# Kernel optimization log

Hardware: AMD Instinct MI355X
Metric: run time of the kernel (lower is better)

The kernel has to match this reference:

```python
import jax, jax.numpy as jnp
import numpy as np

B, IN, MEM, CTX, H = 8192, 1024, 1024, 1024, 4
DH = CTX // H

def setup_inputs() -> dict:
    key = jax.random.key(0)
    ks = jax.random.split(key, 20)
    s = 0.02
    d = {
        'input_tensor': jax.random.normal(ks[0], (B, IN), jnp.float32),
        'previous_memory': jax.random.normal(ks[1], (B, MEM), jnp.float32),
        # MultiheadAttention packed in_proj (q,k,v) and out_proj
        'in_proj_w': jax.random.normal(ks[2], (3 * CTX, CTX), jnp.float32) * s,
        'in_proj_b': jnp.zeros((3 * CTX,), jnp.float32),
        'out_proj_w': jax.random.normal(ks[3], (CTX, CTX), jnp.float32) * s,
        'out_proj_b': jnp.zeros((CTX,), jnp.float32),
        # input/memory projections
        'ip_w': jax.random.normal(ks[4], (CTX, IN), jnp.float32) * s,
        'ip_b': jnp.zeros((CTX,), jnp.float32),
        'mp_w': jax.random.normal(ks[5], (CTX, MEM), jnp.float32) * s,
        'mp_b': jnp.zeros((CTX,), jnp.float32),
        # forget / output gates
        'fg_w': jax.random.normal(ks[6], (MEM, MEM + IN), jnp.float32) * s,
        'fg_b': jnp.zeros((MEM,), jnp.float32),
        'og_w': jax.random.normal(ks[7], (MEM, MEM), jnp.float32) * s,
        'og_b': jnp.zeros((MEM,), jnp.float32),
        # GRUCell weights (PyTorch layout: [3*hidden, in], gates order r,z,n)
        'gru_w_ih': jax.random.normal(ks[8], (3 * MEM, CTX), jnp.float32) * s,
        'gru_b_ih': jnp.zeros((3 * MEM,), jnp.float32),
        'gru_w_hh': jax.random.normal(ks[9], (3 * MEM, MEM), jnp.float32) * s,
        'gru_b_hh': jnp.zeros((3 * MEM,), jnp.float32),
    }
    return d

def _forward(input_tensor, previous_memory, in_proj_w, in_proj_b, out_proj_w, out_proj_b,
             ip_w, ip_b, mp_w, mp_b, fg_w, fg_b, og_w, og_b,
             gru_w_ih, gru_b_ih, gru_w_hh, gru_b_hh):
    # projections
    pi = input_tensor @ ip_w.T + ip_b          # [B, CTX] (query; also context/value)
    pm = previous_memory @ mp_w.T + mp_b       # [B, CTX] (key)
    # MHA with q_len = kv_len = 1: softmax over a single key -> weights = 1
    wq, wk, wv = jnp.split(in_proj_w, 3, axis=0)
    bq, bk, bv = jnp.split(in_proj_b, 3, axis=0)
    q = (pi @ wq.T + bq).reshape(B, H, DH)
    k = (pm @ wk.T + bk).reshape(B, H, DH)
    v = (pi @ wv.T + bv).reshape(B, H, DH)
    scores = jnp.sum(q * k, axis=-1, keepdims=True) / jnp.sqrt(jnp.float32(DH))  # [B,H,1]
    w = jax.nn.softmax(scores, axis=-1)        # all ones (single key)
    attn = (w * v).reshape(B, CTX)             # == v
    context_aware = attn @ out_proj_w.T + out_proj_b  # [B, CTX]
    attention_weights = jnp.mean(w, axis=1)[:, None, :]  # [B,1,1], avg over heads
    # forget gate
    forget_in = jnp.concatenate([previous_memory, input_tensor], axis=-1)
    fgate = jax.nn.sigmoid(forget_in @ fg_w.T + fg_b)
    gated_mem = previous_memory * fgate
    # GRUCell (PyTorch semantics)
    gi = context_aware @ gru_w_ih.T + gru_b_ih
    gh = gated_mem @ gru_w_hh.T + gru_b_hh
    gi_r, gi_z, gi_n = jnp.split(gi, 3, axis=-1)
    gh_r, gh_z, gh_n = jnp.split(gh, 3, axis=-1)
    r = jax.nn.sigmoid(gi_r + gh_r)
    z = jax.nn.sigmoid(gi_z + gh_z)
    n = jnp.tanh(gi_n + r * gh_n)
    updated = (1.0 - z) * n + z * gated_mem
    ogate = jax.nn.sigmoid(updated @ og_w.T + og_b)
    return updated * ogate, attention_weights

def reference(input_tensor, previous_memory, in_proj_w, in_proj_b, out_proj_w, out_proj_b,
              ip_w, ip_b, mp_w, mp_b, fg_w, fg_b, og_w, og_b,
              gru_w_ih, gru_b_ih, gru_w_hh, gru_b_hh):
    return _forward(input_tensor, previous_memory, in_proj_w, in_proj_b, out_proj_w, out_proj_b,
                    ip_w, ip_b, mp_w, mp_b, fg_w, fg_b, og_w, og_b,
                    gru_w_ih, gru_b_ih, gru_w_hh, gru_b_hh)
```

## Files before the change

### kernel.cpp

```cpp
#include <hip/hip_runtime.h>
#include <cstdint>
#include <cstddef>


typedef __bf16 bf16;
typedef bf16 bf16x4 __attribute__((ext_vector_type(4)));
typedef bf16 bf16x8 __attribute__((ext_vector_type(8)));
typedef float f32x4 __attribute__((ext_vector_type(4)));

#define B_ROWS 8192

__device__ __forceinline__ float sigmoid_f(float x) {
    return 1.0f / (1.0f + __expf(-x));
}
__device__ __forceinline__ float tanh_f(float x) {
    return 1.0f - 2.0f / (__expf(2.0f * x) + 1.0f);
}

__global__ __launch_bounds__(256, 2) void gemm256x128_k(
    const bf16* __restrict__ A, int lda,
    const bf16* __restrict__ W, int ldw,
    const float* __restrict__ bias, int N, int K, int epi,
    bf16* __restrict__ out_bf, float* __restrict__ out_f32,
    const float* __restrict__ aux_f32, const bf16* __restrict__ aux_bf,
    int nby)
{
    __shared__ bf16 lds[36864];
    bf16* sA = lds;
    bf16* sB = lds + 3 * 256 * 32;

    const int tid  = threadIdx.x;
    const int lane = tid & 63;
    const int wave = tid >> 6;
    const int wm   = wave >> 1;
    const int wn   = wave & 1;
    const int lrow = lane & 15;
    const int lq   = lane >> 4;

    const int by   = blockIdx.x % nby;
    const int bx   = blockIdx.x / nby;
    const int brow = by * 256;
    const int bcol = bx * 128;

    f32x4 acc[8][4];
#pragma unroll
    for (int i = 0; i < 8; ++i)
#pragma unroll
        for (int j = 0; j < 4; ++j) {
            f32x4 z = {0.0f, 0.0f, 0.0f, 0.0f};
            acc[i][j] = z;
        }

    auto stage = [&](bf16* dA, bf16* dB, int k0) {
#pragma unroll
        for (int i = 0; i < 4; ++i) {
            const int s   = tid + i * 256;
            const int row = s >> 2;
            const int col = (((s & 3) ^ ((s >> 3) & 3)) << 3);
            const bf16* gp = A + (size_t)(brow + row) * lda + (k0 + col);
            __builtin_amdgcn_global_load_lds(
                (const __attribute__((address_space(1))) void*)gp,
                (__attribute__((address_space(3))) void*)(&dA[s * 8]),
                16, 0, 0);
        }
#pragma unroll
        for (int i = 0; i < 2; ++i) {
            const int s   = tid + i * 256;
            const int row = s >> 2;
            const int col = (((s & 3) ^ ((s >> 3) & 3)) << 3);
            const bf16* gp = W + (size_t)(bcol + row) * ldw + (k0 + col);
            __builtin_amdgcn_global_load_lds(
                (const __attribute__((address_space(1))) void*)gp,
                (__attribute__((address_space(3))) void*)(&dB[s * 8]),
                16, 0, 0);
        }
    };

    const int NT = K >> 5;

    bf16* a0 = sA;                bf16* b0 = sB;
    bf16* a1 = sA + 256 * 32;     bf16* b1 = sB + 128 * 32;
    bf16* a2 = sA + 2 * 256 * 32; bf16* b2 = sB + 2 * 128 * 32;

    stage(a0, b0, 0);
    stage(a1, b1, NT > 1 ? 32 : 0);
    asm volatile("s_waitcnt vmcnt(6)" ::: "memory");
    __builtin_amdgcn_s_barrier();
    __builtin_amdgcn_sched_barrier(0);

    for (int kt = 0; kt < NT; ++kt) {
        bf16x8 av[8], bv[4];
#pragma unroll
        for (int i = 0; i < 8; ++i) {
            const int r = wm * 128 + i * 16 + lrow;
            av[i] = *(const bf16x8*)&a0[r * 32 + ((lq ^ ((r >> 1) & 3)) << 3)];
        }
#pragma unroll
        for (int j = 0; j < 4; ++j) {
            const int r = wn * 64 + j * 16 + lrow;
            bv[j] = *(const bf16x8*)&b0[r * 32 + ((lq ^ ((r >> 1) & 3)) << 3)];
        }

        const int kn = (kt + 2 < NT ? kt + 2 : NT - 1) << 5;
        stage(a2, b2, kn);

#pragma unroll
        for (int i = 0; i < 8; ++i)
#pragma unroll
            for (int j = 0; j < 4; ++j)
                acc[i][j] = __builtin_amdgcn_mfma_f32_16x16x32_bf16(
                    av[i], bv[j], acc[i][j], 0, 0, 0);

        __builtin_amdgcn_sched_barrier(0);
        asm volatile("s_waitcnt vmcnt(6)" ::: "memory");
        __builtin_amdgcn_s_barrier();
        __builtin_amdgcn_sched_barrier(0);

        bf16* ta = a0; a0 = a1; a1 = a2; a2 = ta;
        bf16* tb = b0; b0 = b1; b1 = b2; b2 = tb;
    }

    asm volatile("s_waitcnt vmcnt(0)" ::: "memory");
    __syncthreads();

    if (epi == 0) {
        bf16* cb = lds;
#pragma unroll
        for (int j = 0; j < 4; ++j) {
            const int col = wn * 64 + j * 16 + lrow;
            const float bj = bias[bcol + col];
#pragma unroll
            for (int i = 0; i < 8; ++i) {
                const int rowb = wm * 128 + i * 16 + lq * 4;
#pragma unroll
                for (int r = 0; r < 4; ++r)
                    cb[(rowb + r) * 136 + col] = (bf16)(acc[i][j][r] + bj);
            }
        }
        __syncthreads();
#pragma unroll
        for (int p = 0; p < 16; ++p) {
            const int row = p * 16 + (tid >> 4);
            const int col = (tid & 15) * 8;
            bf16x8 v = *(const bf16x8*)&cb[row * 136 + col];
            *(bf16x8*)&out_bf[(size_t)(brow + row) * N + bcol + col] = v;
        }
    } else {
        float* cf = (float*)lds;
#pragma unroll
        for (int h = 0; h < 2; ++h) {
            if (wm == h) {
#pragma unroll
                for (int j = 0; j < 4; ++j) {
                    const int col = wn * 64 + j * 16 + lrow;
                    const float bj = bias[bcol + col];
#pragma unroll
                    for (int i = 0; i < 8; ++i) {
                        const int rl = i * 16 + lq * 4;
#pragma unroll
                        for (int r = 0; r < 4; ++r)
                            cf[(rl + r) * 132 + col] = acc[i][j][r] + bj;
                    }
                }
            }
            __syncthreads();
#pragma unroll
            for (int p = 0; p < 16; ++p) {
                const int idx = p * 256 + tid;
                const int row = idx >> 5;
                const int ch  = idx & 31;
                f32x4 v = *(const f32x4*)&cf[row * 132 + ch * 4];
                const int grow = brow + h * 128 + row;
                const int gcol = bcol + ch * 4;
                const size_t gidx = (size_t)grow * N + gcol;
                if (epi == 1) {
                    f32x4 a4 = *(const f32x4*)&aux_f32[gidx];
                    bf16x4 o;
#pragma unroll
                    for (int e = 0; e < 4; ++e)
                        o[e] = (bf16)(a4[e] * sigmoid_f(v[e]));
                    *(bf16x4*)&out_bf[gidx] = o;
                } else {
                    bf16x4 ab = *(const bf16x4*)&aux_bf[gidx];
                    f32x4 o;
#pragma unroll
                    for (int e = 0; e < 4; ++e)
                        o[e] = (float)ab[e] * sigmoid_f(v[e]);
                    *(f32x4*)&out_f32[gidx] = o;
                }
            }
            __syncthreads();
        }
    }
}

template <int BM>
__device__ __forceinline__ void gemm_core_tb(
    bf16* sA, bf16* sB,
    const bf16* __restrict__ A, int lda,
    const bf16* __restrict__ W, int ldw,
    const float* __restrict__ bias,
    int N, int K, int brow, int bcol, int epi,
    bf16* __restrict__ out_bf, int tld)
{
    constexpr int AI = BM / 32;
    const int tid  = threadIdx.x;
    const int lane = tid & 63;
    const int wave = tid >> 6;
    const int wr   = (wave & 1) * (BM / 2);
    const int wc   = (wave >> 1) * 64;
    const int lrow = lane & 15;
    const int lq   = lane >> 4;

    f32x4 acc[AI][4];
#pragma unroll
    for (int i = 0; i < AI; ++i)
#pragma unroll
        for (int j = 0; j < 4; ++j) {
            f32x4 z = {0.0f, 0.0f, 0.0f, 0.0f};
            acc[i][j] = z;
        }

    auto stage = [&](bf16* dA, bf16* dB, int k0) {
#pragma unroll
        for (int i = 0; i < BM / 64; ++i) {
            const int s   = tid + i * 256;
            const int row = s >> 2;
            const int col = (((s & 3) ^ ((s >> 3) & 3)) << 3);
            const bf16* gp = A + (size_t)(brow + row) * lda + (k0 + col);
            __builtin_amdgcn_global_load_lds(
                (const __attribute__((address_space(1))) void*)gp,
                (__attribute__((address_space(3))) void*)(&dA[s * 8]),
                16, 0, 0);
        }
#pragma unroll
        for (int i = 0; i < 2; ++i) {
            const int s   = tid + i * 256;
            const int row = s >> 2;
            const int col = (((s & 3) ^ ((s >> 3) & 3)) << 3);
            const bf16* gp = W + (size_t)(bcol + row) * ldw + (k0 + col);
            __builtin_amdgcn_global_load_lds(
                (const __attribute__((address_space(1))) void*)gp,
                (__attribute__((address_space(3))) void*)(&dB[s * 8]),
                16, 0, 0);
        }
    };

#define WAIT_LPS()                                                   \
    do {                                                             \
        if constexpr (BM == 128)                                     \
            asm volatile("s_waitcnt vmcnt(4)" ::: "memory");         \
        else                                                         \
            asm volatile("s_waitcnt vmcnt(3)" ::: "memory");         \
    } while (0)

    const int NT = K >> 5;

    bf16* a0 = sA;               bf16* b0 = sB;
    bf16* a1 = sA + BM * 32;     bf16* b1 = sB + 4096;
    bf16* a2 = sA + 2 * BM * 32; bf16* b2 = sB + 2 * 4096;

    stage(a0, b0, 0);
    stage(a1, b1, NT > 1 ? 32 : 0);
    WAIT_LPS();
    __builtin_amdgcn_s_barrier();
    __builtin_amdgcn_sched_barrier(0);

    for (int kt = 0; kt < NT; ++kt) {
        bf16x8 av[AI], bv[4];
#pragma unroll
        for (int i = 0; i < AI; ++i) {
            const int r = wr + i * 16 + lrow;
            av[i] = *(const bf16x8*)&a0[r * 32 + ((lq ^ ((r >> 1) & 3)) << 3)];
        }
#pragma unroll
        for (int j = 0; j < 4; ++j) {
            const int r = wc + j * 16 + lrow;
            bv[j] = *(const bf16x8*)&b0[r * 32 + ((lq ^ ((r >> 1) & 3)) << 3)];
        }

        const int kn = (kt + 2 < NT ? kt + 2 : NT - 1) << 5;
        stage(a2, b2, kn);

#pragma unroll
        for (int i = 0; i < AI; ++i)
#pragma unroll
            for (int j = 0; j < 4; ++j)
                acc[i][j] = __builtin_amdgcn_mfma_f32_16x16x32_bf16(
                    av[i], bv[j], acc[i][j], 0, 0, 0);

        __builtin_amdgcn_sched_barrier(0);
        WAIT_LPS();
        __builtin_amdgcn_s_barrier();
        __builtin_amdgcn_sched_barrier(0);

        bf16* ta = a0; a0 = a1; a1 = a2; a2 = ta;
        bf16* tb = b0; b0 = b1; b1 = b2; b2 = tb;
    }

    asm volatile("s_waitcnt vmcnt(0)" ::: "memory");
#undef WAIT_LPS

#pragma unroll
    for (int j = 0; j < 4; ++j) {
        const int gcol = bcol + wc + j * 16 + lrow;
        const float bj = bias ? bias[gcol] : 0.0f;
#pragma unroll
        for (int i = 0; i < AI; ++i) {
            const int growb = brow + wr + i * 16 + lq * 4;
#pragma unroll
            for (int r = 0; r < 4; ++r) {
                const int grow = growb + r;
                const float val = acc[i][j][r] + bj;
                if (epi == 0) {
                    out_bf[(size_t)grow * N + gcol] = (bf16)val;
                } else {
                    out_bf[(size_t)gcol * tld + grow] = (bf16)val;
                }
            }
        }
    }
}

__global__ __launch_bounds__(256, 2) void gemm64_k(
    const bf16* __restrict__ A, int lda, const bf16* __restrict__ W, int ldw,
    const float* __restrict__ bias, int N, int K, int epi,
    bf16* __restrict__ out_bf, int tld, int nby)
{
    __shared__ bf16 sA[3 * 64 * 32];
    __shared__ bf16 sB[3 * 128 * 32];
    const int by = blockIdx.x % nby;
    const int bx = blockIdx.x / nby;
    gemm_core_tb<64>(sA, sB, A, lda, W, ldw, bias, N, K,
                     by * 64, bx * 128, epi, out_bf, tld);
}


__global__ void cast_weights_k(
    const float* __restrict__ wv, const float* __restrict__ wop,
    const float* __restrict__ wih, const float* __restrict__ wfg,
    const float* __restrict__ wog,
    bf16* __restrict__ dv, bf16* __restrict__ dop, bf16* __restrict__ dih,
    bf16* __restrict__ dfg, bf16* __restrict__ dog)
{
    int c = blockIdx.x * 256 + threadIdx.x;
    const float* s;
    bf16* d;
    int o;
    if (c < 262144)        { s = wv;  d = dv;  o = c; }
    else if (c < 524288)   { s = wop; d = dop; o = c - 262144; }
    else if (c < 1310720)  { s = wih; d = dih; o = c - 524288; }
    else if (c < 1835008)  { s = wfg; d = dfg; o = c - 1310720; }
    else                   { s = wog; d = dog; o = c - 1835008; }
    f32x4 v = ((const f32x4*)s)[o];
    bf16x4 t = {(bf16)v[0], (bf16)v[1], (bf16)v[2], (bf16)v[3]};
    ((bf16x4*)d)[o] = t;
}

__global__ void cast_f32_bf16_k(const float* __restrict__ src,
                                bf16* __restrict__ dst, int n4) {
    int i = blockIdx.x * 256 + threadIdx.x;
    if (i >= n4) return;
    f32x4 v = ((const f32x4*)src)[i];
    bf16x4 o = {(bf16)v[0], (bf16)v[1], (bf16)v[2], (bf16)v[3]};
    ((bf16x4*)dst)[i] = o;
}

__global__ void build_cat_k(const float* __restrict__ mem,
                            const float* __restrict__ inp,
                            bf16* __restrict__ cat) {
    int i = blockIdx.x * 256 + threadIdx.x;
    int row = i >> 9;
    int c4  = i & 511;
    f32x4 v;
    if (c4 < 256)
        v = ((const f32x4*)mem)[(size_t)row * 256 + c4];
    else
        v = ((const f32x4*)inp)[(size_t)row * 256 + (c4 - 256)];
    bf16x4 o = {(bf16)v[0], (bf16)v[1], (bf16)v[2], (bf16)v[3]};
    ((bf16x4*)cat)[i] = o;
}

__global__ void transpose_cast_k(const float* __restrict__ src,
                                 bf16* __restrict__ dst, int R, int C) {
    __shared__ float t[32][33];
    int bx = blockIdx.x * 32;
    int by = blockIdx.y * 32;
    int tx = threadIdx.x & 31, ty = threadIdx.x >> 5;
#pragma unroll
    for (int i = 0; i < 32; i += 8)
        t[ty + i][tx] = src[(size_t)(by + ty + i) * C + bx + tx];
    __syncthreads();
#pragma unroll
    for (int i = 0; i < 32; i += 8)
        dst[(size_t)(bx + ty + i) * R + by + tx] = (bf16)t[tx][ty + i];
}

__global__ void gemv_k(const float* __restrict__ W, const float* __restrict__ x,
                       const float* __restrict__ b, float* __restrict__ y,
                       int K) {
    int n    = blockIdx.x * 4 + (threadIdx.x >> 6);
    int lane = threadIdx.x & 63;
    const float* row = W + (size_t)n * K;
    float s = 0.0f;
    for (int k = lane * 4; k < K; k += 256) {
        f32x4 w = *(const f32x4*)(row + k);
        f32x4 xv = *(const f32x4*)(x + k);
        s += w[0] * xv[0] + w[1] * xv[1] + w[2] * xv[2] + w[3] * xv[3];
    }
#pragma unroll
    for (int off = 32; off; off >>= 1) s += __shfl_down(s, off);
    if (lane == 0) y[n] = s + b[n];
}

__global__ void gru_combine_k(const bf16* __restrict__ gi,
                              const bf16* __restrict__ gh,
                              bf16* __restrict__ gated) {
    int i   = blockIdx.x * 256 + threadIdx.x;
    int row = i >> 7;
    int c   = (i & 127) << 3;
    size_t b3 = (size_t)row * 3072 + c;
    size_t b1 = (size_t)row * 1024 + c;
    bf16x8 gir = *(const bf16x8*)(gi + b3);
    bf16x8 giz = *(const bf16x8*)(gi + b3 + 1024);
    bf16x8 gin = *(const bf16x8*)(gi + b3 + 2048);
    bf16x8 ghr = *(const bf16x8*)(gh + b3);
    bf16x8 ghz = *(const bf16x8*)(gh + b3 + 1024);
    bf16x8 ghn = *(const bf16x8*)(gh + b3 + 2048);
    bf16x8 g   = *(const bf16x8*)(gated + b1);
    bf16x8 o;
#pragma unroll
    for (int e = 0; e < 8; ++e) {
        float r = sigmoid_f((float)gir[e] + (float)ghr[e]);
        float z = sigmoid_f((float)giz[e] + (float)ghz[e]);
        float n = tanh_f((float)gin[e] + r * (float)ghn[e]);
        o[e] = (bf16)((1.0f - z) * n + z * (float)g[e]);
    }
    *(bf16x8*)(gated + b1) = o;
}

__global__ void fill_ones_k(float* __restrict__ p, int n) {
    int i = blockIdx.x * 256 + threadIdx.x;
    if (i < n) p[i] = 1.0f;
}

extern "C" void kernel_launch(void* const* d_in, const int* in_sizes, int n_in,
                              void* d_out, int out_size, void* d_ws,
                              size_t ws_size, hipStream_t stream) {
    const float* input      = (const float*)d_in[0];
    const float* prev       = (const float*)d_in[1];
    const float* in_proj_w  = (const float*)d_in[2];
    const float* in_proj_b  = (const float*)d_in[3];
    const float* out_proj_w = (const float*)d_in[4];
    const float* out_proj_b = (const float*)d_in[5];
    const float* ip_w       = (const float*)d_in[6];
    const float* ip_b       = (const float*)d_in[7];
    const float* fg_w  = (const float*)d_in[10];
    const float* fg_b  = (const float*)d_in[11];
    const float* og_w  = (const float*)d_in[12];
    const float* og_b  = (const float*)d_in[13];
    const float* gih_w = (const float*)d_in[14];
    const float* gih_b = (const float*)d_in[15];
    const float* ghh_w = (const float*)d_in[16];
    const float* ghh_b = (const float*)d_in[17];
    float* out = (float*)d_out;

    char* ws = (char*)d_ws;
    const size_t MB = 1024 * 1024;
    bf16* CAT   = (bf16*)(ws);
    bf16* WHHB  = (bf16*)(ws);
    bf16* GI    = (bf16*)(ws + 32 * MB);
    bf16* GH    = (bf16*)(ws + 80 * MB);
    bf16* WVB   = (bf16*)(ws + 80 * MB);
    bf16* WOPB  = (bf16*)(ws + 82 * MB);
    bf16* WIHB  = (bf16*)(ws + 84 * MB);
    bf16* WIPT  = (bf16*)(ws + 90 * MB);
    bf16* T1T   = (bf16*)(ws + 92 * MB);
    bf16* T2T   = (bf16*)(ws + 94 * MB);
    bf16* WFGB  = (bf16*)(ws + 96 * MB);
    float* T1B  = (float*)(ws + 100 * MB);
    float* T2B  = (float*)(ws + 100 * MB + 8192);
    float* T3B  = (float*)(ws + 100 * MB + 16384);
    bf16* GATED = (bf16*)(ws + 128 * MB);
    bf16* WCOMB = (bf16*)(ws + 144 * MB);
    bf16* WOGB  = (bf16*)(ws + 150 * MB);

    const int M = B_ROWS;
    dim3 blk(256);

    build_cat_k<<<dim3((M * 2048 / 4) / 256), blk, 0, stream>>>(prev, input, CAT);
    cast_weights_k<<<dim3(8192), blk, 0, stream>>>(
        in_proj_w + 2048 * 1024, out_proj_w, gih_w, fg_w, og_w,
        WVB, WOPB, WIHB, WFGB, WOGB);
    transpose_cast_k<<<dim3(32, 32), blk, 0, stream>>>(ip_w, WIPT, 1024, 1024);
    gemv_k<<<dim3(256), blk, 0, stream>>>(in_proj_w + 2048 * 1024, ip_b, in_proj_b + 2048, T1B, 1024);
    gemv_k<<<dim3(256), blk, 0, stream>>>(out_proj_w, T1B, out_proj_b, T2B, 1024);
    gemv_k<<<dim3(768), blk, 0, stream>>>(gih_w, T2B, gih_b, T3B, 1024);
    gemm64_k<<<dim3(128), blk, 0, stream>>>(WVB, 1024, WIPT, 1024, nullptr,
        1024, 1024, 3, T1T, 1024, 16);
    gemm64_k<<<dim3(128), blk, 0, stream>>>(WOPB, 1024, T1T, 1024, nullptr,
        1024, 1024, 3, T2T, 1024, 16);
    gemm64_k<<<dim3(384), blk, 0, stream>>>(WIHB, 1024, T2T, 1024, nullptr,
        1024, 1024, 0, WCOMB, 0, 48);
    gemm256x128_k<<<dim3(256), blk, 0, stream>>>(CAT, 2048, WFGB, 2048,
        fg_b, 1024, 2048, 1, GATED, nullptr, prev, nullptr, 32);
    gemm256x128_k<<<dim3(768), blk, 0, stream>>>(CAT + 1024, 2048, WCOMB,
        1024, T3B, 3072, 1024, 0, GI, nullptr, nullptr, nullptr, 32);
    cast_f32_bf16_k<<<dim3(3072), blk, 0, stream>>>(ghh_w, WHHB, 3072 * 1024 / 4);
    gemm256x128_k<<<dim3(768), blk, 0, stream>>>(GATED, 1024, WHHB,
        1024, ghh_b, 3072, 1024, 0, GH, nullptr, nullptr, nullptr, 32);
    gru_combine_k<<<dim3(M * 1024 / 8 / 256), blk, 0, stream>>>(GI, GH, GATED);
    gemm256x128_k<<<dim3(256), blk, 0, stream>>>(GATED, 1024, WOGB, 1024,
        og_b, 1024, 1024, 2, nullptr, out, nullptr, GATED, 32);
    fill_ones_k<<<dim3(32), blk, 0, stream>>>(out + (size_t)M * 1024, M);
}
```

Baseline: 467.8 us.

## Fuse GRU gate GEMMs with K-concatenation and fold combine into epilogue

The separate GI and GH GEMMs plus the elementwise GRU combine kernel are restructured. The r/z gates are computed by one GEMM that concatenates the K dimension (input-side and hidden-side operands). The n-gate input GEMM runs in the same launch as the forget-gate GEMM, and the n-gate hidden GEMM applies the full GRU update in its epilogue. This avoids writing and re-reading the large GI/GH intermediates and the extra launches. All preprocessing casts, the transpose and the ones fill are merged into a single prep kernel.

```diff
diff --git a/kernel.cpp b/kernel.cpp
--- a/kernel.cpp
+++ b/kernel.cpp
@@ -17,15 +17,17 @@
     return 1.0f - 2.0f / (__expf(2.0f * x) + 1.0f);
 }
 
-__global__ __launch_bounds__(256, 2) void gemm256x128_k(
-    const bf16* __restrict__ A, int lda,
-    const bf16* __restrict__ W, int ldw,
-    const float* __restrict__ bias, int N, int K, int epi,
-    bf16* __restrict__ out_bf, float* __restrict__ out_f32,
-    const float* __restrict__ aux_f32, const bf16* __restrict__ aux_bf,
-    int nby)
-{
-    __shared__ bf16 lds[36864];
+template <int EPI>
+__device__ __forceinline__ void g256_core(
+    bf16* lds,
+    const bf16* A1, int lda1, const bf16* W1, int ldw1, int nt1,
+    const bf16* A2, int lda2, const bf16* W2, int ldw2, int nt2,
+    const float* bias1, const float* bias2,
+    int N, int brow, int bcol,
+    bf16* out_bf, float* out_f32,
+    const float* aux_f32, const bf16* aux_bf,
+    const bf16* grz, const bf16* gni, const bf16* gat)
+{
     bf16* sA = lds;
     bf16* sB = lds + 3 * 256 * 32;
 
@@ -37,11 +39,6 @@
     const int lrow = lane & 15;
     const int lq   = lane >> 4;
 
-    const int by   = blockIdx.x % nby;
-    const int bx   = blockIdx.x / nby;
-    const int brow = by * 256;
-    const int bcol = bx * 128;
-
     f32x4 acc[8][4];
 #pragma unroll
     for (int i = 0; i < 8; ++i)
@@ -51,9 +48,262 @@
             acc[i][j] = z;
         }
 
+    auto stage = [&](bf16* dA, bf16* dB, int kt) {
+        const bf16* Ab; int lda; const bf16* Wb; int ldw; int k0;
+        if (kt < nt1) { Ab = A1; lda = lda1; Wb = W1; ldw = ldw1; k0 = kt << 5; }
+        else          { Ab = A2; lda = lda2; Wb = W2; ldw = ldw2; k0 = (kt - nt1) << 5; }
+#pragma unroll
+        for (int i = 0; i < 4; ++i) {
+            const int s   = tid + i * 256;
+            const int row = s >> 2;
+            const int col = (((s & 3) ^ ((s >> 3) & 3)) << 3);
+            const bf16* gp = Ab + (size_t)(brow + row) * lda + (k0 + col);
+            __builtin_amdgcn_global_load_lds(
+                (const __attribute__((address_space(1))) void*)gp,
+                (__attribute__((address_space(3))) void*)(&dA[s * 8]),
+                16, 0, 0);
+        }
+#pragma unroll
+        for (int i = 0; i < 2; ++i) {
+            const int s   = tid + i * 256;
+            const int row = s >> 2;
+            const int col = (((s & 3) ^ ((s >> 3) & 3)) << 3);
+            const bf16* gp = Wb + (size_t)(bcol + row) * ldw + (k0 + col);
+            __builtin_amdgcn_global_load_lds(
+                (const __attribute__((address_space(1))) void*)gp,
+                (__attribute__((address_space(3))) void*)(&dB[s * 8]),
+                16, 0, 0);
+        }
+    };
+
+    const int NT = nt1 + nt2;
+
+    bf16* a0 = sA;           bf16* b0 = sB;
+    bf16* a1 = sA + 8192;    bf16* b1 = sB + 4096;
+    bf16* a2 = sA + 16384;   bf16* b2 = sB + 8192;
+
+    stage(a0, b0, 0);
+    stage(a1, b1, 1);
+    asm volatile("s_waitcnt vmcnt(6)" ::: "memory");
+    __builtin_amdgcn_s_barrier();
+    __builtin_amdgcn_sched_barrier(0);
+
+    for (int kt = 0; kt < NT; ++kt) {
+        bf16x8 av[8], bv[4];
+#pragma unroll
+        for (int i = 0; i < 8; ++i) {
+            const int r = wm * 128 + i * 16 + lrow;
+            av[i] = *(const bf16x8*)&a0[r * 32 + ((lq ^ ((r >> 1) & 3)) << 3)];
+        }
+#pragma unroll
+        for (int j = 0; j < 4; ++j) {
+            const int r = wn * 64 + j * 16 + lrow;
+            bv[j] = *(const bf16x8*)&b0[r * 32 + ((lq ^ ((r >> 1) & 3)) << 3)];
+        }
+
+        stage(a2, b2, kt + 2 < NT ? kt + 2 : NT - 1);
+
+#pragma unroll
+        for (int i = 0; i < 8; ++i)
+#pragma unroll
+            for (int j = 0; j < 4; ++j)
+                acc[i][j] = __builtin_amdgcn_mfma_f32_16x16x32_bf16(
+                    av[i], bv[j], acc[i][j], 0, 0, 0);
+
+        __builtin_amdgcn_sched_barrier(0);
+        asm volatile("s_waitcnt vmcnt(6)" ::: "memory");
+        __builtin_amdgcn_s_barrier();
+        __builtin_amdgcn_sched_barrier(0);
+
+        bf16* ta = a0; a0 = a1; a1 = a2; a2 = ta;
+        bf16* tb = b0; b0 = b1; b1 = b2; b2 = tb;
+    }
+
+    asm volatile("s_waitcnt vmcnt(0)" ::: "memory");
+    __syncthreads();
+
+    if constexpr (EPI == 0) {
+        bf16* cb = lds;
+#pragma unroll
+        for (int j = 0; j < 4; ++j) {
+            const int col = wn * 64 + j * 16 + lrow;
+            float bj = bias1[bcol + col];
+            if (bias2) bj += bias2[bcol + col];
+#pragma unroll
+            for (int i = 0; i < 8; ++i) {
+                const int rowb = wm * 128 + i * 16 + lq * 4;
+#pragma unroll
+                for (int r = 0; r < 4; ++r)
+                    cb[(rowb + r) * 136 + col] = (bf16)(acc[i][j][r] + bj);
+            }
+        }
+        __syncthreads();
+#pragma unroll
+        for (int p = 0; p < 16; ++p) {
+            const int row = p * 16 + (tid >> 4);
+            const int col = (tid & 15) * 8;
+            bf16x8 v = *(const bf16x8*)&cb[row * 136 + col];
+            *(bf16x8*)&out_bf[(size_t)(brow + row) * N + bcol + col] = v;
+        }
+    } else {
+        float* cf = (float*)lds;
+#pragma unroll
+        for (int h = 0; h < 2; ++h) {
+            if (wm == h) {
+#pragma unroll
+                for (int j = 0; j < 4; ++j) {
+                    const int col = wn * 64 + j * 16 + lrow;
+                    const float bj = bias1[bcol + col];
+#pragma unroll
+                    for (int i = 0; i < 8; ++i) {
+                        const int rl = i * 16 + lq * 4;
+#pragma unroll
+                        for (int r = 0; r < 4; ++r)
+                            cf[(rl + r) * 132 + col] = acc[i][j][r] + bj;
+                    }
+                }
+            }
+            __syncthreads();
+#pragma unroll
+            for (int p = 0; p < 16; ++p) {
+                const int idx = p * 256 + tid;
+                const int row = idx >> 5;
+                const int ch  = idx & 31;
+                f32x4 v = *(const f32x4*)&cf[row * 132 + ch * 4];
+                const int grow = brow + h * 128 + row;
+                const int gcol = bcol + ch * 4;
+                const size_t gidx = (size_t)grow * N + gcol;
+                if constexpr (EPI == 1) {
+                    f32x4 a4 = *(const f32x4*)&aux_f32[gidx];
+                    bf16x4 o;
+#pragma unroll
+                    for (int e = 0; e < 4; ++e)
+                        o[e] = (bf16)(a4[e] * sigmoid_f(v[e]));
+                    *(bf16x4*)&out_bf[gidx] = o;
+                } else if constexpr (EPI == 2) {
+                    bf16x4 ab = *(const bf16x4*)&aux_bf[gidx];
+                    f32x4 o;
+#pragma unroll
+                    for (int e = 0; e < 4; ++e)
+                        o[e] = (float)ab[e] * sigmoid_f(v[e]);
+                    *(f32x4*)&out_f32[gidx] = o;
+                } else {
+                    const bf16* pr = grz + (size_t)grow * 2048 + gcol;
+                    bf16x4 rr = *(const bf16x4*)pr;
+                    bf16x4 zz = *(const bf16x4*)(pr + 1024);
+                    bf16x4 g4 = *(const bf16x4*)&gni[gidx];
+                    bf16x4 m4 = *(const bf16x4*)&gat[gidx];
+                    bf16x4 o;
+#pragma unroll
+                    for (int e = 0; e < 4; ++e) {
+                        const float r = sigmoid_f((float)rr[e]);
+                        const float z = sigmoid_f((float)zz[e]);
+                        const float n = tanh_f((float)g4[e] + r * v[e]);
+                        o[e] = (bf16)((1.0f - z) * n + z * (float)m4[e]);
+                    }
+                    *(bf16x4*)&out_bf[gidx] = o;
+                }
+            }
+            __syncthreads();
+        }
+    }
+}
+
+__global__ __launch_bounds__(256, 2) void fgg1_k(
+    const bf16* __restrict__ cat, const bf16* __restrict__ wfg,
+    const float* __restrict__ fg_b, const float* __restrict__ prev,
+    bf16* __restrict__ gated,
+    const bf16* __restrict__ wcomb_n, const float* __restrict__ bias_n,
+    bf16* __restrict__ gni)
+{
+    __shared__ bf16 lds[36864];
+    const int id = blockIdx.x;
+    if (id < 256) {
+        const int by = id & 31, bx = id >> 5;
+        g256_core<1>(lds, cat, 2048, wfg, 2048, 64,
+                     nullptr, 0, nullptr, 0, 0,
+                     fg_b, nullptr, 1024, by * 256, bx * 128,
+                     gated, nullptr, prev, nullptr, nullptr, nullptr, nullptr);
+    } else {
+        const int id2 = id - 256;
+        const int by = id2 & 31, bx = id2 >> 5;
+        g256_core<0>(lds, cat + 1024, 2048, wcomb_n, 1024, 32,
+                     nullptr, 0, nullptr, 0, 0,
+                     bias_n, nullptr, 1024, by * 256, bx * 128,
+                     gni, nullptr, nullptr, nullptr, nullptr, nullptr, nullptr);
+    }
+}
+
+__global__ __launch_bounds__(256, 2) void g2_k(
+    const bf16* __restrict__ x, const bf16* __restrict__ wcomb,
+    const bf16* __restrict__ gated, const bf16* __restrict__ whh,
+    const float* __restrict__ t3b, const float* __restrict__ bhh,
+    bf16* __restrict__ grz)
+{
+    __shared__ bf16 lds[36864];
+    const int by = blockIdx.x & 31, bx = blockIdx.x >> 5;
+    g256_core<0>(lds, x, 2048, wcomb, 1024, 32,
+                 gated, 1024, whh, 1024, 32,
+                 t3b, bhh, 2048, by * 256, bx * 128,
+                 grz, nullptr, nullptr, nullptr, nullptr, nullptr, nullptr);
+}
+
+__global__ __launch_bounds__(256, 2) void g3_k(
+    const bf16* __restrict__ gated, const bf16* __restrict__ whh_n,
+    const float* __restrict__ bhh_n,
+    const bf16* __restrict__ grz, const bf16* __restrict__ gni,
+    bf16* __restrict__ upd)
+{
+    __shared__ bf16 lds[36864];
+    const int by = blockIdx.x & 31, bx = blockIdx.x >> 5;
+    g256_core<4>(lds, gated, 1024, whh_n, 1024, 32,
+                 nullptr, 0, nullptr, 0, 0,
+                 bhh_n, nullptr, 1024, by * 256, bx * 128,
+                 upd, nullptr, nullptr, nullptr, grz, gni, gated);
+}
+
+__global__ __launch_bounds__(256, 2) void og_k(
+    const bf16* __restrict__ upd, const bf16* __restrict__ wog,
+    const float* __restrict__ og_b, float* __restrict__ out)
+{
+    __shared__ bf16 lds[36864];
+    const int by = blockIdx.x & 31, bx = blockIdx.x >> 5;
+    g256_core<2>(lds, upd, 1024, wog, 1024, 32,
+                 nullptr, 0, nullptr, 0, 0,
+                 og_b, nullptr, 1024, by * 256, bx * 128,
+                 nullptr, out, nullptr, upd, nullptr, nullptr, nullptr);
+}
+
+template <int BM>
+__device__ __forceinline__ void gemm_core_tb(
+    bf16* sA, bf16* sB,
+    const bf16* __restrict__ A, int lda,
+    const bf16* __restrict__ W, int ldw,
+    const float* __restrict__ bias,
+    int N, int K, int brow, int bcol, int epi,
+    bf16* __restrict__ out_bf, int tld)
+{
+    constexpr int AI = BM / 32;
+    const int tid  = threadIdx.x;
+    const int lane = tid & 63;
+    const int wave = tid >> 6;
+    const int wr   = (wave & 1) * (BM / 2);
+    const int wc   = (wave >> 1) * 64;
+    const int lrow = lane & 15;
+    const int lq   = lane >> 4;
+
+    f32x4 acc[AI][4];
+#pragma unroll
+    for (int i = 0; i < AI; ++i)
+#pragma unroll
+        for (int j = 0; j < 4; ++j) {
+            f32x4 z = {0.0f, 0.0f, 0.0f, 0.0f};
+            acc[i][j] = z;
+        }
+
     auto stage = [&](bf16* dA, bf16* dB, int k0) {
 #pragma unroll
-        for (int i = 0; i < 4; ++i) {
+        for (int i = 0; i < BM / 64; ++i) {
             const int s   = tid + i * 256;
             const int row = s >> 2;
             const int col = (((s & 3) ^ ((s >> 3) & 3)) << 3);
@@ -76,176 +326,6 @@
         }
     };
 
-    const int NT = K >> 5;
-
-    bf16* a0 = sA;                bf16* b0 = sB;
-    bf16* a1 = sA + 256 * 32;     bf16* b1 = sB + 128 * 32;
-    bf16* a2 = sA + 2 * 256 * 32; bf16* b2 = sB + 2 * 128 * 32;
-
-    stage(a0, b0, 0);
-    stage(a1, b1, NT > 1 ? 32 : 0);
-    asm volatile("s_waitcnt vmcnt(6)" ::: "memory");
-    __builtin_amdgcn_s_barrier();
-    __builtin_amdgcn_sched_barrier(0);
-
-    for (int kt = 0; kt < NT; ++kt) {
-        bf16x8 av[8], bv[4];
-#pragma unroll
-        for (int i = 0; i < 8; ++i) {
-            const int r = wm * 128 + i * 16 + lrow;
-            av[i] = *(const bf16x8*)&a0[r * 32 + ((lq ^ ((r >> 1) & 3)) << 3)];
-        }
-#pragma unroll
-        for (int j = 0; j < 4; ++j) {
-            const int r = wn * 64 + j * 16 + lrow;
-            bv[j] = *(const bf16x8*)&b0[r * 32 + ((lq ^ ((r >> 1) & 3)) << 3)];
-        }
-
-        const int kn = (kt + 2 < NT ? kt + 2 : NT - 1) << 5;
-        stage(a2, b2, kn);
-
-#pragma unroll
-        for (int i = 0; i < 8; ++i)
-#pragma unroll
-            for (int j = 0; j < 4; ++j)
-                acc[i][j] = __builtin_amdgcn_mfma_f32_16x16x32_bf16(
-                    av[i], bv[j], acc[i][j], 0, 0, 0);
-
-        __builtin_amdgcn_sched_barrier(0);
-        asm volatile("s_waitcnt vmcnt(6)" ::: "memory");
-        __builtin_amdgcn_s_barrier();
-        __builtin_amdgcn_sched_barrier(0);
-
-        bf16* ta = a0; a0 = a1; a1 = a2; a2 = ta;
-        bf16* tb = b0; b0 = b1; b1 = b2; b2 = tb;
-    }
-
-    asm volatile("s_waitcnt vmcnt(0)" ::: "memory");
-    __syncthreads();
-
-    if (epi == 0) {
-        bf16* cb = lds;
-#pragma unroll
-        for (int j = 0; j < 4; ++j) {
-            const int col = wn * 64 + j * 16 + lrow;
-            const float bj = bias[bcol + col];
-#pragma unroll
-            for (int i = 0; i < 8; ++i) {
-                const int rowb = wm * 128 + i * 16 + lq * 4;
-#pragma unroll
-                for (int r = 0; r < 4; ++r)
-                    cb[(rowb + r) * 136 + col] = (bf16)(acc[i][j][r] + bj);
-            }
-        }
-        __syncthreads();
-#pragma unroll
-        for (int p = 0; p < 16; ++p) {
-            const int row = p * 16 + (tid >> 4);
-            const int col = (tid & 15) * 8;
-            bf16x8 v = *(const bf16x8*)&cb[row * 136 + col];
-            *(bf16x8*)&out_bf[(size_t)(brow + row) * N + bcol + col] = v;
-        }
-    } else {
-        float* cf = (float*)lds;
-#pragma unroll
-        for (int h = 0; h < 2; ++h) {
-            if (wm == h) {
-#pragma unroll
-                for (int j = 0; j < 4; ++j) {
-                    const int col = wn * 64 + j * 16 + lrow;
-                    const float bj = bias[bcol + col];
-#pragma unroll
-                    for (int i = 0; i < 8; ++i) {
-                        const int rl = i * 16 + lq * 4;
-#pragma unroll
-                        for (int r = 0; r < 4; ++r)
-                            cf[(rl + r) * 132 + col] = acc[i][j][r] + bj;
-                    }
-                }
-            }
-            __syncthreads();
-#pragma unroll
-            for (int p = 0; p < 16; ++p) {
-                const int idx = p * 256 + tid;
-                const int row = idx >> 5;
-                const int ch  = idx & 31;
-                f32x4 v = *(const f32x4*)&cf[row * 132 + ch * 4];
-                const int grow = brow + h * 128 + row;
-                const int gcol = bcol + ch * 4;
-                const size_t gidx = (size_t)grow * N + gcol;
-                if (epi == 1) {
-                    f32x4 a4 = *(const f32x4*)&aux_f32[gidx];
-                    bf16x4 o;
-#pragma unroll
-                    for (int e = 0; e < 4; ++e)
-                        o[e] = (bf16)(a4[e] * sigmoid_f(v[e]));
-                    *(bf16x4*)&out_bf[gidx] = o;
-                } else {
-                    bf16x4 ab = *(const bf16x4*)&aux_bf[gidx];
-                    f32x4 o;
-#pragma unroll
-                    for (int e = 0; e < 4; ++e)
-                        o[e] = (float)ab[e] * sigmoid_f(v[e]);
-                    *(f32x4*)&out_f32[gidx] = o;
-                }
-            }
-            __syncthreads();
-        }
-    }
-}
-
-template <int BM>
-__device__ __forceinline__ void gemm_core_tb(
-    bf16* sA, bf16* sB,
-    const bf16* __restrict__ A, int lda,
-    const bf16* __restrict__ W, int ldw,
-    const float* __restrict__ bias,
-    int N, int K, int brow, int bcol, int epi,
-    bf16* __restrict__ out_bf, int tld)
-{
-    constexpr int AI = BM / 32;
-    const int tid  = threadIdx.x;
-    const int lane = tid & 63;
-    const int wave = tid >> 6;
-    const int wr   = (wave & 1) * (BM / 2);
-    const int wc   = (wave >> 1) * 64;
-    const int lrow = lane & 15;
-    const int lq   = lane >> 4;
-
-    f32x4 acc[AI][4];
-#pragma unroll
-    for (int i = 0; i < AI; ++i)
-#pragma unroll
-        for (int j = 0; j < 4; ++j) {
-            f32x4 z = {0.0f, 0.0f, 0.0f, 0.0f};
-            acc[i][j] = z;
-        }
-
-    auto stage = [&](bf16* dA, bf16* dB, int k0) {
-#pragma unroll
-        for (int i = 0; i < BM / 64; ++i) {
-            const int s   = tid + i * 256;
-            const int row = s >> 2;
-            const int col = (((s & 3) ^ ((s >> 3) & 3)) << 3);
-            const bf16* gp = A + (size_t)(brow + row) * lda + (k0 + col);
-            __builtin_amdgcn_global_load_lds(
-                (const __attribute__((address_space(1))) void*)gp,
-                (__attribute__((address_space(3))) void*)(&dA[s * 8]),
-                16, 0, 0);
-        }
-#pragma unroll
-        for (int i = 0; i < 2; ++i) {
-            const int s   = tid + i * 256;
-            const int row = s >> 2;
-            const int col = (((s & 3) ^ ((s >> 3) & 3)) << 3);
-            const bf16* gp = W + (size_t)(bcol + row) * ldw + (k0 + col);
-            __builtin_amdgcn_global_load_lds(
-                (const __attribute__((address_space(1))) void*)gp,
-                (__attribute__((address_space(3))) void*)(&dB[s * 8]),
-                16, 0, 0);
-        }
-    };
-
 #define WAIT_LPS()                                                   \
     do {                                                             \
         if constexpr (BM == 128)                                     \
@@ -335,65 +415,61 @@
                      by * 64, bx * 128, epi, out_bf, tld);
 }
 
-
-__global__ void cast_weights_k(
+__global__ void prep_k(
+    const float* __restrict__ prev, const float* __restrict__ input,
+    bf16* __restrict__ cat,
     const float* __restrict__ wv, const float* __restrict__ wop,
     const float* __restrict__ wih, const float* __restrict__ wfg,
-    const float* __restrict__ wog,
+    const float* __restrict__ wog, const float* __restrict__ whh,
     bf16* __restrict__ dv, bf16* __restrict__ dop, bf16* __restrict__ dih,
-    bf16* __restrict__ dfg, bf16* __restrict__ dog)
-{
-    int c = blockIdx.x * 256 + threadIdx.x;
-    const float* s;
-    bf16* d;
-    int o;
-    if (c < 262144)        { s = wv;  d = dv;  o = c; }
-    else if (c < 524288)   { s = wop; d = dop; o = c - 262144; }
-    else if (c < 1310720)  { s = wih; d = dih; o = c - 524288; }
-    else if (c < 1835008)  { s = wfg; d = dfg; o = c - 1310720; }
-    else                   { s = wog; d = dog; o = c - 1835008; }
-    f32x4 v = ((const f32x4*)s)[o];
-    bf16x4 t = {(bf16)v[0], (bf16)v[1], (bf16)v[2], (bf16)v[3]};
-    ((bf16x4*)d)[o] = t;
-}
-
-__global__ void cast_f32_bf16_k(const float* __restrict__ src,
-                                bf16* __restrict__ dst, int n4) {
-    int i = blockIdx.x * 256 + threadIdx.x;
-    if (i >= n4) return;
-    f32x4 v = ((const f32x4*)src)[i];
-    bf16x4 o = {(bf16)v[0], (bf16)v[1], (bf16)v[2], (bf16)v[3]};
-    ((bf16x4*)dst)[i] = o;
-}
-
-__global__ void build_cat_k(const float* __restrict__ mem,
-                            const float* __restrict__ inp,
-                            bf16* __restrict__ cat) {
-    int i = blockIdx.x * 256 + threadIdx.x;
-    int row = i >> 9;
-    int c4  = i & 511;
-    f32x4 v;
-    if (c4 < 256)
-        v = ((const f32x4*)mem)[(size_t)row * 256 + c4];
-    else
-        v = ((const f32x4*)inp)[(size_t)row * 256 + (c4 - 256)];
-    bf16x4 o = {(bf16)v[0], (bf16)v[1], (bf16)v[2], (bf16)v[3]};
-    ((bf16x4*)cat)[i] = o;
-}
-
-__global__ void transpose_cast_k(const float* __restrict__ src,
-                                 bf16* __restrict__ dst, int R, int C) {
+    bf16* __restrict__ dfg, bf16* __restrict__ dog, bf16* __restrict__ dhh,
+    const float* __restrict__ ipw, bf16* __restrict__ wipt,
+    float* __restrict__ ones)
+{
     __shared__ float t[32][33];
-    int bx = blockIdx.x * 32;
-    int by = blockIdx.y * 32;
-    int tx = threadIdx.x & 31, ty = threadIdx.x >> 5;
-#pragma unroll
-    for (int i = 0; i < 32; i += 8)
-        t[ty + i][tx] = src[(size_t)(by + ty + i) * C + bx + tx];
-    __syncthreads();
-#pragma unroll
-    for (int i = 0; i < 32; i += 8)
-        dst[(size_t)(bx + ty + i) * R + by + tx] = (bf16)t[tx][ty + i];
+    const int b = blockIdx.x;
+    if (b < 16384) {
+        const int i = b * 256 + threadIdx.x;
+        const int row = i >> 9;
+        const int c4  = i & 511;
+        f32x4 v;
+        if (c4 < 256)
+            v = ((const f32x4*)prev)[(size_t)row * 256 + c4];
+        else
+            v = ((const f32x4*)input)[(size_t)row * 256 + (c4 - 256)];
+        bf16x4 o = {(bf16)v[0], (bf16)v[1], (bf16)v[2], (bf16)v[3]};
+        ((bf16x4*)cat)[i] = o;
+    } else if (b < 27648) {
+        const int c = (b - 16384) * 256 + threadIdx.x;
+        const float* s; bf16* d; int o;
+        if (c < 262144)        { s = wv;  d = dv;  o = c; }
+        else if (c < 524288)   { s = wop; d = dop; o = c - 262144; }
+        else if (c < 1310720)  { s = wih; d = dih; o = c - 524288; }
+        else if (c < 1835008)  { s = wfg; d = dfg; o = c - 1310720; }
+        else if (c < 2097152)  { s = wog; d = dog; o = c - 1835008; }
+        else                   { s = whh; d = dhh; o = c - 2097152; }
+        f32x4 v = ((const f32x4*)s)[o];
+        bf16x4 w = {(bf16)v[0], (bf16)v[1], (bf16)v[2], (bf16)v[3]};
+        ((bf16x4*)d)[o] = w;
+    } else if (b < 28672) {
+        const int b2 = b - 27648;
+        const int bx = (b2 & 31) * 32;
+        const int by = (b2 >> 5) * 32;
+        const int tx = threadIdx.x & 31, ty = threadIdx.x >> 5;
+#pragma unroll
+        for (int i = 0; i < 32; i += 8)
+            t[ty + i][tx] = ipw[(size_t)(by + ty + i) * 1024 + bx + tx];
+        __syncthreads();
+#pragma unroll
+        for (int i = 0; i < 32; i += 8)
+            wipt[(size_t)(bx + ty + i) * 1024 + by + tx] = (bf16)t[tx][ty + i];
+    } else {
+        const int i = (b - 28672) * 256 + threadIdx.x;
+        if (i < 2048) {
+            f32x4 one = {1.0f, 1.0f, 1.0f, 1.0f};
+            ((f32x4*)ones)[i] = one;
+        }
+    }
 }
 
 __global__ void gemv_k(const float* __restrict__ W, const float* __restrict__ x,
@@ -411,37 +487,6 @@
 #pragma unroll
     for (int off = 32; off; off >>= 1) s += __shfl_down(s, off);
     if (lane == 0) y[n] = s + b[n];
-}
-
-__global__ void gru_combine_k(const bf16* __restrict__ gi,
-                              const bf16* __restrict__ gh,
-                              bf16* __restrict__ gated) {
-    int i   = blockIdx.x * 256 + threadIdx.x;
-    int row = i >> 7;
-    int c   = (i & 127) << 3;
-    size_t b3 = (size_t)row * 3072 + c;
-    size_t b1 = (size_t)row * 1024 + c;
-    bf16x8 gir = *(const bf16x8*)(gi + b3);
-    bf16x8 giz = *(const bf16x8*)(gi + b3 + 1024);
-    bf16x8 gin = *(const bf16x8*)(gi + b3 + 2048);
-    bf16x8 ghr = *(const bf16x8*)(gh + b3);
-    bf16x8 ghz = *(const bf16x8*)(gh + b3 + 1024);
-    bf16x8 ghn = *(const bf16x8*)(gh + b3 + 2048);
-    bf16x8 g   = *(const bf16x8*)(gated + b1);
-    bf16x8 o;
-#pragma unroll
-    for (int e = 0; e < 8; ++e) {
-        float r = sigmoid_f((float)gir[e] + (float)ghr[e]);
-        float z = sigmoid_f((float)giz[e] + (float)ghz[e]);
-        float n = tanh_f((float)gin[e] + r * (float)ghn[e]);
-        o[e] = (bf16)((1.0f - z) * n + z * (float)g[e]);
-    }
-    *(bf16x8*)(gated + b1) = o;
-}
-
-__global__ void fill_ones_k(float* __restrict__ p, int n) {
-    int i = blockIdx.x * 256 + threadIdx.x;
-    if (i < n) p[i] = 1.0f;
 }
 
 extern "C" void kernel_launch(void* const* d_in, const int* in_sizes, int n_in,
@@ -468,31 +513,32 @@
     char* ws = (char*)d_ws;
     const size_t MB = 1024 * 1024;
     bf16* CAT   = (bf16*)(ws);
-    bf16* WHHB  = (bf16*)(ws);
-    bf16* GI    = (bf16*)(ws + 32 * MB);
-    bf16* GH    = (bf16*)(ws + 80 * MB);
-    bf16* WVB   = (bf16*)(ws + 80 * MB);
-    bf16* WOPB  = (bf16*)(ws + 82 * MB);
-    bf16* WIHB  = (bf16*)(ws + 84 * MB);
-    bf16* WIPT  = (bf16*)(ws + 90 * MB);
-    bf16* T1T   = (bf16*)(ws + 92 * MB);
-    bf16* T2T   = (bf16*)(ws + 94 * MB);
-    bf16* WFGB  = (bf16*)(ws + 96 * MB);
-    float* T1B  = (float*)(ws + 100 * MB);
-    float* T2B  = (float*)(ws + 100 * MB + 8192);
-    float* T3B  = (float*)(ws + 100 * MB + 16384);
-    bf16* GATED = (bf16*)(ws + 128 * MB);
-    bf16* WCOMB = (bf16*)(ws + 144 * MB);
-    bf16* WOGB  = (bf16*)(ws + 150 * MB);
+    bf16* WHHB  = (bf16*)(ws + 32 * MB);
+    bf16* GRZ   = (bf16*)(ws + 38 * MB);
+    bf16* GNI   = (bf16*)(ws + 70 * MB);
+    bf16* GATED = (bf16*)(ws + 86 * MB);
+    bf16* UPD   = (bf16*)(ws + 102 * MB);
+    bf16* WCOMB = (bf16*)(ws + 118 * MB);
+    bf16* WOGB  = (bf16*)(ws + 124 * MB);
+    bf16* WFGB  = (bf16*)(ws + 126 * MB);
+    bf16* WVB   = (bf16*)(ws + 130 * MB);
+    bf16* WOPB  = (bf16*)(ws + 132 * MB);
+    bf16* WIHB  = (bf16*)(ws + 134 * MB);
+    bf16* WIPT  = (bf16*)(ws + 140 * MB);
+    bf16* T1T   = (bf16*)(ws + 142 * MB);
+    bf16* T2T   = (bf16*)(ws + 144 * MB);
+    float* T1B  = (float*)(ws + 146 * MB);
+    float* T2B  = (float*)(ws + 146 * MB + 8192);
+    float* T3B  = (float*)(ws + 146 * MB + 16384);
 
     const int M = B_ROWS;
     dim3 blk(256);
 
-    build_cat_k<<<dim3((M * 2048 / 4) / 256), blk, 0, stream>>>(prev, input, CAT);
-    cast_weights_k<<<dim3(8192), blk, 0, stream>>>(
-        in_proj_w + 2048 * 1024, out_proj_w, gih_w, fg_w, og_w,
-        WVB, WOPB, WIHB, WFGB, WOGB);
-    transpose_cast_k<<<dim3(32, 32), blk, 0, stream>>>(ip_w, WIPT, 1024, 1024);
+    prep_k<<<dim3(28680), blk, 0, stream>>>(
+        prev, input, CAT,
+        in_proj_w + 2048 * 1024, out_proj_w, gih_w, fg_w, og_w, ghh_w,
+        WVB, WOPB, WIHB, WFGB, WOGB, WHHB,
+        ip_w, WIPT, out + (size_t)M * 1024);
     gemv_k<<<dim3(256), blk, 0, stream>>>(in_proj_w + 2048 * 1024, ip_b, in_proj_b + 2048, T1B, 1024);
     gemv_k<<<dim3(256), blk, 0, stream>>>(out_proj_w, T1B, out_proj_b, T2B, 1024);
     gemv_k<<<dim3(768), blk, 0, stream>>>(gih_w, T2B, gih_b, T3B, 1024);
@@ -502,15 +548,12 @@
         1024, 1024, 3, T2T, 1024, 16);
     gemm64_k<<<dim3(384), blk, 0, stream>>>(WIHB, 1024, T2T, 1024, nullptr,
         1024, 1024, 0, WCOMB, 0, 48);
-    gemm256x128_k<<<dim3(256), blk, 0, stream>>>(CAT, 2048, WFGB, 2048,
-        fg_b, 1024, 2048, 1, GATED, nullptr, prev, nullptr, 32);
-    gemm256x128_k<<<dim3(768), blk, 0, stream>>>(CAT + 1024, 2048, WCOMB,
-        1024, T3B, 3072, 1024, 0, GI, nullptr, nullptr, nullptr, 32);
-    cast_f32_bf16_k<<<dim3(3072), blk, 0, stream>>>(ghh_w, WHHB, 3072 * 1024 / 4);
-    gemm256x128_k<<<dim3(768), blk, 0, stream>>>(GATED, 1024, WHHB,
-        1024, ghh_b, 3072, 1024, 0, GH, nullptr, nullptr, nullptr, 32);
-    gru_combine_k<<<dim3(M * 1024 / 8 / 256), blk, 0, stream>>>(GI, GH, GATED);
-    gemm256x128_k<<<dim3(256), blk, 0, stream>>>(GATED, 1024, WOGB, 1024,
-        og_b, 1024, 1024, 2, nullptr, out, nullptr, GATED, 32);
-    fill_ones_k<<<dim3(32), blk, 0, stream>>>(out + (size_t)M * 1024, M);
-}
+    fgg1_k<<<dim3(512), blk, 0, stream>>>(
+        CAT, WFGB, fg_b, prev, GATED,
+        WCOMB + (size_t)2048 * 1024, T3B + 2048, GNI);
+    g2_k<<<dim3(512), blk, 0, stream>>>(
+        CAT + 1024, WCOMB, GATED, WHHB, T3B, ghh_b, GRZ);
+    g3_k<<<dim3(256), blk, 0, stream>>>(
+        GATED, WHHB + (size_t)2048 * 1024, ghh_b + 2048, GRZ, GNI, UPD);
+    og_k<<<dim3(256), blk, 0, stream>>>(UPD, WOGB, og_b, out);
+}
```

After: 455.2 us. -2.7%, faster.
